# Kernel tuning notes

Hardware: AMD Instinct MI355X
Metric: run time of the kernel (lower is better)

The kernel has to match this reference:

```python
import jax, jax.numpy as jnp
import numpy as np

N_NODES = 20000
N_GRAPH = 256
NODE_DIM = 128
MULS = (128, 64, 32)       # node irreps: 128x0e + 64x1o + 32x2e
HC = 32                    # hidden channels per irrep
HIDDEN_DIM = 64
N_PATH = 9                 # feasible uuw paths into 0e+1e+2e
W_NUMEL = N_PATH * HC * HC # 9216


def _tables():
    # real Clebsch-Gordan tensors built from cartesian tensor algebra,
    # normalized so that sum(C**2) = 2*l_out + 1 (component normalization)
    eps = np.zeros((3, 3, 3))
    eps[0, 1, 2] = eps[1, 2, 0] = eps[2, 0, 1] = 1.0
    eps[0, 2, 1] = eps[2, 1, 0] = eps[1, 0, 2] = -1.0
    s2, s6 = 1 / np.sqrt(2), 1 / np.sqrt(6)
    Q2 = np.zeros((5, 3, 3))  # orthonormal basis of traceless symmetric 3x3
    Q2[0, 0, 1] = Q2[0, 1, 0] = s2          # xy
    Q2[1, 1, 2] = Q2[1, 2, 1] = s2          # yz
    Q2[2, 0, 0] = Q2[2, 1, 1] = -s6; Q2[2, 2, 2] = 2 * s6  # z2
    Q2[3, 0, 2] = Q2[3, 2, 0] = s2          # xz
    Q2[4, 0, 0] = s2; Q2[4, 1, 1] = -s2     # x2-y2

    def nrm(C, l3):
        return C * np.sqrt((2 * l3 + 1) / (C ** 2).sum())

    C000 = np.ones((1, 1, 1))
    C022 = np.eye(5)[None, :, :]
    C110 = np.eye(3).reshape(3, 3, 1) / np.sqrt(3)
    C111 = eps / np.sqrt(2)
    C112 = np.transpose(Q2, (1, 2, 0))
    C202 = np.eye(5)[:, None, :]
    C220 = np.eye(5).reshape(5, 5, 1) / np.sqrt(5)
    M = np.einsum('iab,jdb->ijad', Q2, Q2)  # [5,5,3,3]
    C221 = nrm(np.einsum('cad,ijad->ijc', eps, M), 1)
    S = 0.5 * (M + np.transpose(M, (0, 1, 3, 2)))
    S = S - np.trace(S, axis1=2, axis2=3)[..., None, None] * np.eye(3) / 3.0
    C222 = nrm(np.einsum('kad,ijad->ijk', Q2, S), 2)
    # sph2cart change of basis: 9 spherical comps (0e+1e+2e) -> 3x3 cartesian
    Qc = np.zeros((3, 3, 9))
    Qc[:, :, 0] = np.eye(3) / np.sqrt(3)        # isotropic part
    Qc[:, :, 1:4] = eps / np.sqrt(2)            # antisymmetric part
    Qc[:, :, 4:9] = np.transpose(Q2, (1, 2, 0)) # symmetric traceless part
    return [C000, C022, C110, C111, C112, C202, C220, C221, C222], Qc

_CGS, _QC = _tables()


def setup_inputs() -> dict:
    key = jax.random.key(0)
    ks = jax.random.split(key, 12)
    f32 = jnp.float32
    d_sph = MULS[0] + 3 * MULS[1] + 5 * MULS[2]  # 480
    return {
        'x_scalar': jax.random.normal(ks[0], (N_NODES, NODE_DIM), f32),
        'x_spherical': jax.random.normal(ks[1], (N_NODES, d_sph), f32),
        'batch': jnp.sort(jax.random.randint(ks[2], (N_NODES,), 0, N_GRAPH)),
        'W0e': jax.random.normal(ks[3], (MULS[0], HC), f32),
        'W1o': jax.random.normal(ks[4], (MULS[1], HC), f32),
        'W2e': jax.random.normal(ks[5], (MULS[2], HC), f32),
        'Wm1': jax.random.normal(ks[6], (NODE_DIM, HIDDEN_DIM), f32) / np.sqrt(NODE_DIM),
        'bm1': jnp.zeros((HIDDEN_DIM,), f32),
        'Wm2': jax.random.normal(ks[7], (HIDDEN_DIM, W_NUMEL), f32) / np.sqrt(HIDDEN_DIM),
        'bm2': jnp.zeros((W_NUMEL,), f32),
        'P0': jax.random.normal(ks[8], (3 * HC,), f32),
        'P1': jax.random.normal(ks[9], (2 * HC,), f32),
        'P2': jax.random.normal(ks[10], (4 * HC,), f32),
    }


def reference(x_scalar, x_spherical, batch, W0e, W1o, W2e, Wm1, bm1, Wm2, bm2, P0, P1, P2):
    n = x_scalar.shape[0]
    m0, m1, m2 = MULS
    # split node features into irrep blocks
    x0 = x_spherical[:, :m0, None]                        # [N,128,1] 0e
    x1 = x_spherical[:, m0:m0 + 3 * m1].reshape(n, m1, 3) # [N,64,3]  1o
    x2 = x_spherical[:, m0 + 3 * m1:].reshape(n, m2, 5)   # [N,32,5]  2e
    # pre_lin: per-irrep channel mixing (e3nn-style 1/sqrt(fan_in))
    h = [jnp.einsum('num,uv->nvm', x, W) / np.sqrt(W.shape[0])
         for x, W in ((x0, W0e), (x1, W1o), (x2, W2e))]   # each [N,32,2l+1]
    # per-node tensor-product weights from scalar features
    w = (jax.nn.silu(x_scalar @ Wm1 + bm1) @ Wm2 + bm2).reshape(n, N_PATH, HC, HC)
    # uuw tensor product, path order matches _CGS
    paths = ((0, 0), (0, 2), (1, 1), (1, 1), (1, 1), (2, 0), (2, 2), (2, 2), (2, 2))
    inv_u = 1.0 / np.sqrt(HC)
    outs = []
    for k, (i, j) in enumerate(paths):
        C = jnp.asarray(_CGS[k], x_scalar.dtype)
        outs.append(jnp.einsum('pqr,nup,nuq,nuw->nwr', C, h[i], h[j], w[:, k]) * inv_u)
    # post_lin: combine paths of each output l into a single channel
    y0 = jnp.einsum('num,u->nm', jnp.concatenate([outs[0], outs[2], outs[6]], 1), P0) / np.sqrt(3 * HC)
    y1 = jnp.einsum('num,u->nm', jnp.concatenate([outs[3], outs[7]], 1), P1) / np.sqrt(2 * HC)
    y2 = jnp.einsum('num,u->nm', jnp.concatenate([outs[1], outs[4], outs[5], outs[8]], 1), P2) / np.sqrt(4 * HC)
    sph = jnp.concatenate([y0, y1, y2], axis=1)           # [N,9]
    cart = jnp.einsum('abi,ni->nab', jnp.asarray(_QC, sph.dtype), sph)  # [N,3,3]
    red = jax.ops.segment_sum(cart, batch, num_segments=N_GRAPH)        # [B,3,3]
    # if_trace is False (if_iso=False): roll every non-batch dim by 1
    return jnp.roll(jnp.roll(red, 1, axis=1), 1, axis=2)
```

## Files before the change

kernel.cpp:

```cpp
#include <hip/hip_runtime.h>
#include <math.h>

#define OFF_W2P 0
#define OFF_B2P 14336
#define WS_FLOATS 14592

#define SC_Y0 0.0180421959121758f
#define SC_Y2 0.015625f
#define S2f 0.70710678118654752f
#define S6f 0.40824829046386302f
#define TWOS2f 1.41421356237309505f
#define TWOS6f 0.81649658092772603f
#define ISQRT3 0.57735026918962576f
#define ISQRT5 0.44721359549995794f
#define H0SC 0.08838834764831845f
#define H1SC 0.125f
#define H2SC 0.17677669529663689f

__device__ __constant__ int KARR[7] = {0, 1, 2, 4, 5, 6, 8};

__global__ __launch_bounds__(256) void prep_kernel(
    const float* __restrict__ Wm2, const float* __restrict__ bm2,
    const float* __restrict__ P0, const float* __restrict__ P2,
    float* __restrict__ ws, float* __restrict__ out) {
  int j = blockIdx.x * 256 + threadIdx.x;
  if (j < 2304) out[j] = 0.f;

  if (j < 14336) {
    int s = j >> 11; int rem = j & 2047; int c = rem >> 5; int u = rem & 31;
    int k = KARR[s];
    const float* P;
    float sc;
    switch (s) {
      case 0: P = P0;      sc = SC_Y0; break;
      case 1: P = P2;      sc = SC_Y2; break;
      case 2: P = P0 + 32; sc = SC_Y0; break;
      case 3: P = P2 + 32; sc = SC_Y2; break;
      case 4: P = P2 + 64; sc = SC_Y2; break;
      case 5: P = P0 + 64; sc = SC_Y0; break;
      default: P = P2 + 96; sc = SC_Y2; break;
    }
    const float4* w4 = (const float4*)(Wm2 + c * 9216 + k * 1024 + u * 32);
    const float4* p4 = (const float4*)P;
    float acc = 0.f;
#pragma unroll
    for (int q = 0; q < 8; ++q) {
      float4 a = w4[q], b = p4[q];
      acc += a.x * b.x + a.y * b.y + a.z * b.z + a.w * b.w;
    }
    ws[OFF_W2P + c * 224 + s * 32 + u] = acc * sc;
  } else if (j < 14560) {
    int i = j - 14336; int s = i >> 5; int u = i & 31; int k = KARR[s];
    const float* P;
    float sc;
    switch (s) {
      case 0: P = P0;      sc = SC_Y0; break;
      case 1: P = P2;      sc = SC_Y2; break;
      case 2: P = P0 + 32; sc = SC_Y0; break;
      case 3: P = P2 + 32; sc = SC_Y2; break;
      case 4: P = P2 + 64; sc = SC_Y2; break;
      case 5: P = P0 + 64; sc = SC_Y0; break;
      default: P = P2 + 96; sc = SC_Y2; break;
    }
    const float* b = bm2 + k * 1024 + u * 32;
    float acc = 0.f;
#pragma unroll
    for (int w = 0; w < 32; ++w) acc += b[w] * P[w];
    ws[OFF_B2P + s * 32 + u] = acc * sc;
  }
}

__global__ __launch_bounds__(256, 6) void fused_kernel(
    const float* __restrict__ xs_g, const float* __restrict__ xsph,
    const float* __restrict__ W0e, const float* __restrict__ W1o,
    const float* __restrict__ W2e,
    const float* __restrict__ Wm1, const float* __restrict__ bm1,
    const float* __restrict__ ws, const int* __restrict__ batch,
    float* __restrict__ out, const float norm2) {
  __shared__ __align__(16) float smem[6384];
  float (*xp)[484] = (float (*)[484])smem;
  float (*xs)[132] = (float (*)[132])(smem + 3872);
  float (*Vt)[228] = (float (*)[228])(smem + 3872);
  float (*hiT)[10] = (float (*)[10])(smem + 5696);
  float (*sphs)[6] = (float (*)[6])(smem + 6336);

  const int tid = threadIdx.x;
  const int n0 = blockIdx.x * 8;

  for (int idx = tid; idx < 1216; idx += 256) {
    if (idx < 960) {
      const int row = idx / 120, c4 = idx % 120;
      *(float4*)&xp[row][c4 * 4] = *(const float4*)(xsph + (size_t)(n0 + row) * 480 + c4 * 4);
    } else {
      const int j = idx - 960;
      const int row = j >> 5, c4 = j & 31;
      *(float4*)&xs[row][c4 * 4] = *(const float4*)(xs_g + (size_t)(n0 + row) * 128 + c4 * 4);
    }
  }
  __syncthreads();

  {
    const int n = tid >> 5, c0 = (tid & 31) * 2;
    float acc0 = 0.f, acc1 = 0.f;
#pragma unroll 4
    for (int mq = 0; mq < 32; ++mq) {
      const float4 xv = *(float4*)&xs[n][mq * 4];
      const float xa[4] = {xv.x, xv.y, xv.z, xv.w};
#pragma unroll
      for (int r = 0; r < 4; ++r) {
        const float2 w = *(const float2*)(Wm1 + (mq * 4 + r) * 64 + c0);
        acc0 += xa[r] * w.x;
        acc1 += xa[r] * w.y;
      }
    }
    const float z0 = acc0 + bm1[c0];
    const float z1 = acc1 + bm1[c0 + 1];
    hiT[c0][n] = z0 / (1.f + __expf(-z0));
    hiT[c0 + 1][n] = z1 / (1.f + __expf(-z1));
  }
  __syncthreads();

  if (tid < 224) {
    const int o = tid;
    float acc[8];
    const float b = ws[OFF_B2P + o];
#pragma unroll
    for (int n = 0; n < 8; ++n) acc[n] = b;
#pragma unroll 4
    for (int c = 0; c < 64; ++c) {
      const float w = ws[OFF_W2P + c * 224 + o];
#pragma unroll
      for (int n = 0; n < 8; ++n) acc[n] += hiT[c][n] * w;
    }
#pragma unroll
    for (int n = 0; n < 8; ++n) Vt[n][o] = acc[n];
  }

  const int u = tid & 31, ni = tid >> 5;
  const float* row = xp[ni];

  float h0;
  {
    float a0 = 0.f;
#pragma unroll 4
    for (int mq = 0; mq < 32; ++mq) {
      const float4 xv = *(const float4*)(row + mq * 4);
      const float xa[4] = {xv.x, xv.y, xv.z, xv.w};
#pragma unroll
      for (int r = 0; r < 4; ++r) a0 += xa[r] * W0e[(mq * 4 + r) * 32 + u];
    }
    h0 = a0 * H0SC;
  }

  float h1a, h1b, h1c;
  {
    float a1[3] = {0.f, 0.f, 0.f};
#pragma unroll 2
    for (int mq = 0; mq < 16; ++mq) {
      const float4 b0 = *(const float4*)(row + 128 + mq * 12);
      const float4 b1 = *(const float4*)(row + 128 + mq * 12 + 4);
      const float4 b2 = *(const float4*)(row + 128 + mq * 12 + 8);
      const float xa[12] = {b0.x, b0.y, b0.z, b0.w, b1.x, b1.y, b1.z, b1.w,
                            b2.x, b2.y, b2.z, b2.w};
#pragma unroll
      for (int mm = 0; mm < 4; ++mm) {
        const float w = W1o[(mq * 4 + mm) * 32 + u];
#pragma unroll
        for (int j = 0; j < 3; ++j) a1[j] += xa[mm * 3 + j] * w;
      }
    }
    h1a = a1[0] * H1SC; h1b = a1[1] * H1SC; h1c = a1[2] * H1SC;
  }

  float h2v[5];
  {
    float a2[5] = {0.f, 0.f, 0.f, 0.f, 0.f};
#pragma unroll 2
    for (int mq = 0; mq < 8; ++mq) {
      const float4 c0v = *(const float4*)(row + 320 + mq * 20);
      const float4 c1v = *(const float4*)(row + 320 + mq * 20 + 4);
      const float4 c2v = *(const float4*)(row + 320 + mq * 20 + 8);
      const float4 c3v = *(const float4*)(row + 320 + mq * 20 + 12);
      const float4 c4v = *(const float4*)(row + 320 + mq * 20 + 16);
      const float xa[20] = {c0v.x, c0v.y, c0v.z, c0v.w, c1v.x, c1v.y, c1v.z, c1v.w,
                            c2v.x, c2v.y, c2v.z, c2v.w, c3v.x, c3v.y, c3v.z, c3v.w,
                            c4v.x, c4v.y, c4v.z, c4v.w};
#pragma unroll
      for (int mm = 0; mm < 4; ++mm) {
        const float w = W2e[(mq * 4 + mm) * 32 + u];
#pragma unroll
        for (int j = 0; j < 5; ++j) a2[j] += xa[mm * 5 + j] * w;
      }
    }
#pragma unroll
    for (int j = 0; j < 5; ++j) h2v[j] = a2[j] * H2SC;
  }
  __syncthreads();

  {
    const float* Vp = &Vt[ni][u];
    const float v0 = Vp[0], v1 = Vp[32], v2 = Vp[64], v3 = Vp[96];
    const float v4 = Vp[128], v5 = Vp[160], v6 = Vp[192];

    const float d11 = h1a * h1a + h1b * h1b + h1c * h1c;
    const float d22 = h2v[0] * h2v[0] + h2v[1] * h2v[1] + h2v[2] * h2v[2] +
                      h2v[3] * h2v[3] + h2v[4] * h2v[4];
    float y0 = v0 * h0 * h0 + v2 * d11 * ISQRT3 + v5 * d22 * ISQRT5;

    const float o00 = h1a * h1a, o01 = h1a * h1b, o02 = h1a * h1c;
    const float o11 = h1b * h1b, o12 = h1b * h1c, o22 = h1c * h1c;
    const float t40 = TWOS2f * o01, t41 = TWOS2f * o12;
    const float t42 = S6f * (2.f * o22 - o00 - o11);
    const float t43 = TWOS2f * o02, t44 = S2f * (o00 - o11);

    const float A00 = -S6f * h2v[2] + S2f * h2v[4];
    const float A01 = S2f * h2v[0];
    const float A02 = S2f * h2v[3];
    const float A11 = -S6f * h2v[2] - S2f * h2v[4];
    const float A12 = S2f * h2v[1];
    const float A22 = TWOS6f * h2v[2];
    const float B00 = A00 * A00 + A01 * A01 + A02 * A02;
    const float B01 = A00 * A01 + A01 * A11 + A02 * A12;
    const float B02 = A00 * A02 + A01 * A12 + A02 * A22;
    const float B11 = A01 * A01 + A11 * A11 + A12 * A12;
    const float B12 = A01 * A02 + A11 * A12 + A12 * A22;
    const float B22 = A02 * A02 + A12 * A12 + A22 * A22;
    const float t80 = TWOS2f * B01, t81 = TWOS2f * B12;
    const float t82 = S6f * (2.f * B22 - B00 - B11);
    const float t83 = TWOS2f * B02, t84 = S2f * (B00 - B11);

    const float w15 = (v1 + v4) * h0;
    const float v6n = v6 * norm2;
    float y2r[5];
    y2r[0] = w15 * h2v[0] + v3 * t40 + v6n * t80;
    y2r[1] = w15 * h2v[1] + v3 * t41 + v6n * t81;
    y2r[2] = w15 * h2v[2] + v3 * t42 + v6n * t82;
    y2r[3] = w15 * h2v[3] + v3 * t43 + v6n * t83;
    y2r[4] = w15 * h2v[4] + v3 * t44 + v6n * t84;

#pragma unroll
    for (int off = 16; off > 0; off >>= 1) {
      y0 += __shfl_xor(y0, off, 32);
#pragma unroll
      for (int r = 0; r < 5; ++r) y2r[r] += __shfl_xor(y2r[r], off, 32);
    }

    if (u == 0) {
      sphs[ni][0] = y0;
#pragma unroll
      for (int r = 0; r < 5; ++r) sphs[ni][1 + r] = y2r[r];
    }
  }
  __syncthreads();

  if (tid < 9) {
    const float QW[9][6] = {
        {ISQRT3, 0.f, 0.f, -S6f, 0.f, S2f},
        {0.f, S2f, 0.f, 0.f, 0.f, 0.f},
        {0.f, 0.f, 0.f, 0.f, S2f, 0.f},
        {0.f, S2f, 0.f, 0.f, 0.f, 0.f},
        {ISQRT3, 0.f, 0.f, -S6f, 0.f, -S2f},
        {0.f, 0.f, S2f, 0.f, 0.f, 0.f},
        {0.f, 0.f, 0.f, 0.f, S2f, 0.f},
        {0.f, 0.f, S2f, 0.f, 0.f, 0.f},
        {ISQRT3, 0.f, 0.f, TWOS6f, 0.f, 0.f}};
    const int a = tid / 3, b = tid % 3;
    const int rolled = ((a + 1) % 3) * 3 + ((b + 1) % 3);
    const float c0 = QW[tid][0], c1 = QW[tid][1], c2 = QW[tid][2];
    const float c3 = QW[tid][3], c4 = QW[tid][4], c5 = QW[tid][5];
    int cur_g = batch[n0];
    float acc = 0.f;
#pragma unroll
    for (int q = 0; q < 8; ++q) {
      const int g = batch[n0 + q];
      const float val = c0 * sphs[q][0] + c1 * sphs[q][1] + c2 * sphs[q][2] +
                        c3 * sphs[q][3] + c4 * sphs[q][4] + c5 * sphs[q][5];
      if (g != cur_g) {
        atomicAdd(out + cur_g * 9 + rolled, acc);
        acc = 0.f;
        cur_g = g;
      }
      acc += val;
    }
    atomicAdd(out + cur_g * 9 + rolled, acc);
  }
}

extern "C" void kernel_launch(void* const* d_in, const int* in_sizes, int n_in,
                              void* d_out, int out_size, void* d_ws, size_t ws_size,
                              hipStream_t stream) {
  const float* x_scalar = (const float*)d_in[0];
  const float* x_sph    = (const float*)d_in[1];
  const int*   batch    = (const int*)d_in[2];
  const float* W0e      = (const float*)d_in[3];
  const float* W1o      = (const float*)d_in[4];
  const float* W2e      = (const float*)d_in[5];
  const float* Wm1      = (const float*)d_in[6];
  const float* bm1      = (const float*)d_in[7];
  const float* Wm2      = (const float*)d_in[8];
  const float* bm2      = (const float*)d_in[9];
  const float* P0       = (const float*)d_in[10];
  const float* P2       = (const float*)d_in[12];
  float* ws  = (float*)d_ws;
  float* out = (float*)d_out;

  if (ws_size < (size_t)WS_FLOATS * sizeof(float)) return;

  double Q2[5][3][3] = {};
  const double s2d = 0.70710678118654752440, s6d = 0.40824829046386301637;
  Q2[0][0][1] = Q2[0][1][0] = s2d;
  Q2[1][1][2] = Q2[1][2][1] = s2d;
  Q2[2][0][0] = Q2[2][1][1] = -s6d; Q2[2][2][2] = 2.0 * s6d;
  Q2[3][0][2] = Q2[3][2][0] = s2d;
  Q2[4][0][0] = s2d; Q2[4][1][1] = -s2d;
  double ss = 0.0;
  for (int i = 0; i < 5; ++i)
    for (int jj = 0; jj < 5; ++jj) {
      double S[3][3];
      for (int a = 0; a < 3; ++a)
        for (int d = 0; d < 3; ++d) {
          double m1 = 0, m2 = 0;
          for (int b = 0; b < 3; ++b) {
            m1 += Q2[i][a][b] * Q2[jj][d][b];
            m2 += Q2[i][d][b] * Q2[jj][a][b];
          }
          S[a][d] = 0.5 * (m1 + m2);
        }
      double tr = (S[0][0] + S[1][1] + S[2][2]) / 3.0;
      S[0][0] -= tr; S[1][1] -= tr; S[2][2] -= tr;
      for (int kk = 0; kk < 5; ++kk) {
        double cc = 0;
        for (int a = 0; a < 3; ++a)
          for (int d = 0; d < 3; ++d) cc += Q2[kk][a][d] * S[a][d];
        ss += cc * cc;
      }
    }
  const float norm2 = (float)sqrt(5.0 / ss);

  prep_kernel<<<57, 256, 0, stream>>>(Wm2, bm2, P0, P2, ws, out);
  fused_kernel<<<2500, 256, 0, stream>>>(x_scalar, x_sph, W0e, W1o, W2e,
                                         Wm1, bm1, ws, batch, out, norm2);
}
```

Before: 170.1 us.

## Read node features directly from global memory and shrink shared memory for occupancy

Drops the cooperative staging of x_spherical and x_scalar into shared memory and has each thread read its node row straight from global memory, which roughly triples down the LDS footprint. The launch-bounds occupancy hint rises from 6 to 8 blocks. The hidden activations are stored node-major so the second MLP layer can read them with float4 loads. In exchange, the per-thread row reads hit global or L1 repeatedly instead of LDS, since all 32 lanes of a node read the same addresses, and one block-wide sync is removed.

```diff
diff --git a/kernel.cpp b/kernel.cpp
--- a/kernel.cpp
+++ b/kernel.cpp
@@ -70,41 +70,28 @@
   }
 }
 
-__global__ __launch_bounds__(256, 6) void fused_kernel(
+__global__ __launch_bounds__(256, 8) void fused_kernel(
     const float* __restrict__ xs_g, const float* __restrict__ xsph,
     const float* __restrict__ W0e, const float* __restrict__ W1o,
     const float* __restrict__ W2e,
     const float* __restrict__ Wm1, const float* __restrict__ bm1,
     const float* __restrict__ ws, const int* __restrict__ batch,
     float* __restrict__ out, const float norm2) {
-  __shared__ __align__(16) float smem[6384];
-  float (*xp)[484] = (float (*)[484])smem;
-  float (*xs)[132] = (float (*)[132])(smem + 3872);
-  float (*Vt)[228] = (float (*)[228])(smem + 3872);
-  float (*hiT)[10] = (float (*)[10])(smem + 5696);
-  float (*sphs)[6] = (float (*)[6])(smem + 6336);
+  __shared__ __align__(16) float smem[2384];
+  float (*Vt)[228] = (float (*)[228])smem;
+  float (*hi2)[64] = (float (*)[64])(smem + 1824);
+  float (*sphs)[6] = (float (*)[6])(smem + 2336);
 
   const int tid = threadIdx.x;
   const int n0 = blockIdx.x * 8;
 
-  for (int idx = tid; idx < 1216; idx += 256) {
-    if (idx < 960) {
-      const int row = idx / 120, c4 = idx % 120;
-      *(float4*)&xp[row][c4 * 4] = *(const float4*)(xsph + (size_t)(n0 + row) * 480 + c4 * 4);
-    } else {
-      const int j = idx - 960;
-      const int row = j >> 5, c4 = j & 31;
-      *(float4*)&xs[row][c4 * 4] = *(const float4*)(xs_g + (size_t)(n0 + row) * 128 + c4 * 4);
-    }
-  }
-  __syncthreads();
-
   {
     const int n = tid >> 5, c0 = (tid & 31) * 2;
+    const float* xr = xs_g + (size_t)(n0 + n) * 128;
     float acc0 = 0.f, acc1 = 0.f;
 #pragma unroll 4
     for (int mq = 0; mq < 32; ++mq) {
-      const float4 xv = *(float4*)&xs[n][mq * 4];
+      const float4 xv = *(const float4*)(xr + mq * 4);
       const float xa[4] = {xv.x, xv.y, xv.z, xv.w};
 #pragma unroll
       for (int r = 0; r < 4; ++r) {
@@ -115,8 +102,8 @@
     }
     const float z0 = acc0 + bm1[c0];
     const float z1 = acc1 + bm1[c0 + 1];
-    hiT[c0][n] = z0 / (1.f + __expf(-z0));
-    hiT[c0 + 1][n] = z1 / (1.f + __expf(-z1));
+    hi2[n][c0] = z0 / (1.f + __expf(-z0));
+    hi2[n][c0 + 1] = z1 / (1.f + __expf(-z1));
   }
   __syncthreads();
 
@@ -127,17 +114,26 @@
 #pragma unroll
     for (int n = 0; n < 8; ++n) acc[n] = b;
 #pragma unroll 4
-    for (int c = 0; c < 64; ++c) {
-      const float w = ws[OFF_W2P + c * 224 + o];
-#pragma unroll
-      for (int n = 0; n < 8; ++n) acc[n] += hiT[c][n] * w;
+    for (int c = 0; c < 64; c += 4) {
+      float4 h4[8];
+#pragma unroll
+      for (int n = 0; n < 8; ++n) h4[n] = *(float4*)&hi2[n][c];
+#pragma unroll
+      for (int r = 0; r < 4; ++r) {
+        const float w = ws[OFF_W2P + (c + r) * 224 + o];
+#pragma unroll
+        for (int n = 0; n < 8; ++n) {
+          const float h = (r == 0) ? h4[n].x : (r == 1) ? h4[n].y : (r == 2) ? h4[n].z : h4[n].w;
+          acc[n] += h * w;
+        }
+      }
     }
 #pragma unroll
     for (int n = 0; n < 8; ++n) Vt[n][o] = acc[n];
   }
 
   const int u = tid & 31, ni = tid >> 5;
-  const float* row = xp[ni];
+  const float* row = xsph + (size_t)(n0 + ni) * 480;
 
   float h0;
   {
```

Result: slower. 214.5 us (+26.1%).
